# Performance work log

Measured on AMD Instinct MI355X. Metric: run time of the kernel, lower is better.

Reference implementation:

```python
import jax, jax.numpy as jnp
import numpy as np

NUM_ITER = 3  # Newton-Schulz iterations (init kwarg)

def setup_inputs() -> dict:
    key = jax.random.key(0)
    x = jax.random.normal(key, (64, 28, 28, 256), dtype=jnp.float32)
    return {"x": x}

def reference(x):
    B, H, W, C = x.shape
    n = H * W
    # Faithful to K.reshape(inputs, (batch, C, n)) -- a plain row-major reshape
    X = x.reshape(B, C, n)
    # Sigma = X @ I_hat @ X^T with I_hat = (1/n)(I - (1/n) 11^T), i.e. the
    # centering projector: identical to mean-centering then (1/n) Xc Xc^T.
    Xc = X - X.mean(axis=2, keepdims=True)            # [B, C, n]
    Sigma = jnp.einsum('bcn,bdn->bcd', Xc, Xc) / n    # [B, C, C]
    trace = jnp.trace(Sigma, axis1=1, axis2=2)[:, None, None]  # [B,1,1]
    A = Sigma / trace
    I = jnp.eye(C, dtype=x.dtype)
    I3 = 3.0 * I
    Y = A
    Z = jnp.broadcast_to(I, (B, C, C))
    # Newton-Schulz: NOTE original updates Z with the already-updated Y
    for _ in range(NUM_ITER):
        Y = 0.5 * jnp.matmul(Y, I3 - jnp.matmul(Z, Y))
        Z = 0.5 * jnp.matmul(I3 - jnp.matmul(Z, Y), Z)
    Cmat = jnp.sqrt(trace) * Y                        # [B, C, C]
    # Upper-triangular (incl. diagonal) vectorization, row-major order
    iu_r, iu_c = jnp.triu_indices(C)
    return Cmat[:, iu_r, iu_c]                        # [B, C*(C+1)/2]
```

## Files before the change

### kernel.cpp

```cpp
#include <hip/hip_runtime.h>
#include <math.h>

#define BATCH 64
#define CD 256
#define NX 784
#define TRIU_N 32896
#define MSZ 65536
#define REG_STRIDE 1032
#define ARR_STRIDE 4128
#define BUF_STRIDE 16512

typedef unsigned short ushort_t;
typedef unsigned int uint_t;
typedef __attribute__((ext_vector_type(8))) short short8;
typedef __attribute__((ext_vector_type(8))) unsigned short ushort8;
typedef __attribute__((ext_vector_type(16))) float floatx16;

__device__ __forceinline__ ushort_t f2bf(float x) {
    uint_t u = __float_as_uint(x);
    u += 0x7fffu + ((u >> 16) & 1u);
    return (ushort_t)(u >> 16);
}
__device__ __forceinline__ float bf2f(ushort_t h) {
    return __uint_as_float(((uint_t)h) << 16);
}
__device__ __forceinline__ void split2(float x, ushort_t& h, ushort_t& l) {
    h = f2bf(x);
    l = f2bf(x - bf2f(h));
}

__device__ __forceinline__ int swoff(int r, int c) {
    int p = r >> 7, s = (c >> 5) & 7, ks = (c >> 4) & 1, kh = (c >> 3) & 1;
    return ((((p * 8 + s) * 2 + ks) * 2 + kh) * 128 + (r & 127)) * 8 + (c & 7);
}

__device__ __forceinline__ void rawbar() {
    __builtin_amdgcn_s_barrier();
    __builtin_amdgcn_sched_barrier(0);
}

__device__ __forceinline__ void mfma_stage8(const ushort_t* us, int bufbase,
                                            int wr, int wcp, int khalf, int lrow,
                                            floatx16* acc) {
    __builtin_amdgcn_s_setprio(1);
    #pragma unroll
    for (int ks = 0; ks < 2; ++ks) {
        const int rid = ks * 2 + khalf;
        const ushort_t* rb = us + bufbase + rid * REG_STRIDE + lrow * 8;
        short8 aH = *(const short8*)(rb + wr * 256);
        short8 aL = *(const short8*)(rb + ARR_STRIDE + wr * 256);
        #pragma unroll
        for (int cq = 0; cq < 2; ++cq) {
            const int col = wcp * 2 + cq;
            short8 bH = *(const short8*)(rb + 2 * ARR_STRIDE + col * 256);
            short8 bL = *(const short8*)(rb + 3 * ARR_STRIDE + col * 256);
            acc[cq] = __builtin_amdgcn_mfma_f32_32x32x16_bf16(aH, bH, acc[cq], 0, 0, 0);
            acc[cq] = __builtin_amdgcn_mfma_f32_32x32x16_bf16(aH, bL, acc[cq], 0, 0, 0);
            acc[cq] = __builtin_amdgcn_mfma_f32_32x32x16_bf16(aL, bH, acc[cq], 0, 0, 0);
        }
    }
    __builtin_amdgcn_s_setprio(0);
}

__device__ __forceinline__ void acc_bounce(float* fsmem, const floatx16* acc,
                                           int wr, int wcp, int khalf, int lrow) {
    __syncthreads();
    #pragma unroll
    for (int cq = 0; cq < 2; ++cq)
        #pragma unroll
        for (int i = 0; i < 16; ++i) {
            int rl = (i & 3) + ((i >> 2) << 3) + (khalf << 2);
            fsmem[(wr * 32 + rl) * 129 + (wcp * 2 + cq) * 32 + lrow] = acc[cq][i];
        }
    __syncthreads();
}

__global__ __launch_bounds__(512, 1)
void gram_mfma(const float* __restrict__ X, float* __restrict__ means,
               ushort_t* __restrict__ Gh, ushort_t* __restrict__ Gl) {
    __shared__ __align__(16) float fsmem[16512];
    ushort_t* us = (ushort_t*)fsmem;
    const int bb = blockIdx.y, tile = blockIdx.x;
    const int rowBase = (tile >> 1) * 128, colBase = (tile & 1) * 128;
    const int tid = threadIdx.x, lane = tid & 63, wv = tid >> 6;
    const int wr = wv >> 1, wcp = wv & 1;
    const int khalf = lane >> 5, lrow = lane & 31;
    const float* Xb = X + (size_t)bb * CD * NX;

    floatx16 acc[2];
    #pragma unroll
    for (int cq = 0; cq < 2; ++cq)
        #pragma unroll
        for (int i = 0; i < 16; ++i) acc[cq][i] = 0.f;

    int side[2], srow[2], skq[2];
    #pragma unroll
    for (int q = 0; q < 2; ++q) {
        int gid = q * 512 + tid;
        side[q] = gid >> 9;
        srow[q] = (gid >> 2) & 127;
        skq[q]  = gid & 3;
    }
    float rs[2] = {0.f, 0.f};

    float4 cur[2][2];
    #pragma unroll
    for (int q = 0; q < 2; ++q) {
        int gk = skq[q] * 8;
        const float* p = Xb + (size_t)((side[q] ? colBase : rowBase) + srow[q]) * NX + gk;
        cur[q][0] = *(const float4*)p;
        cur[q][1] = *(const float4*)(p + 4);
    }
    #pragma unroll
    for (int q = 0; q < 2; ++q) {
        float f[8] = {cur[q][0].x, cur[q][0].y, cur[q][0].z, cur[q][0].w,
                      cur[q][1].x, cur[q][1].y, cur[q][1].z, cur[q][1].w};
        rs[q] += ((f[0] + f[1]) + (f[2] + f[3])) + ((f[4] + f[5]) + (f[6] + f[7]));
        uint_t hp[4], lp[4];
        #pragma unroll
        for (int i = 0; i < 4; ++i) {
            ushort_t h0, l0, h1, l1;
            split2(f[2*i], h0, l0); split2(f[2*i+1], h1, l1);
            hp[i] = (uint_t)h0 | ((uint_t)h1 << 16);
            lp[i] = (uint_t)l0 | ((uint_t)l1 << 16);
        }
        int base = (side[q] * 2) * ARR_STRIDE + skq[q] * REG_STRIDE + srow[q] * 8;
        *(uint4*)(us + base)              = make_uint4(hp[0], hp[1], hp[2], hp[3]);
        *(uint4*)(us + base + ARR_STRIDE) = make_uint4(lp[0], lp[1], lp[2], lp[3]);
    }

    for (int s = 0; s < 25; ++s) {
        asm volatile("s_waitcnt lgkmcnt(0)" ::: "memory");
        rawbar();
        bool more = (s < 24);
        if (more) {
            #pragma unroll
            for (int q = 0; q < 2; ++q) {
                int gk = (s + 1) * 32 + skq[q] * 8;
                if (gk < NX) {
                    const float* p = Xb + (size_t)((side[q] ? colBase : rowBase) + srow[q]) * NX + gk;
                    cur[q][0] = *(const float4*)p;
                    cur[q][1] = *(const float4*)(p + 4);
                } else {
                    cur[q][0] = make_float4(0.f, 0.f, 0.f, 0.f);
                    cur[q][1] = make_float4(0.f, 0.f, 0.f, 0.f);
                }
            }
        }
        mfma_stage8(us, (s & 1) * BUF_STRIDE, wr, wcp, khalf, lrow, acc);
        if (more) {
            int buf = (s + 1) & 1;
            #pragma unroll
            for (int q = 0; q < 2; ++q) {
                float f[8] = {cur[q][0].x, cur[q][0].y, cur[q][0].z, cur[q][0].w,
                              cur[q][1].x, cur[q][1].y, cur[q][1].z, cur[q][1].w};
                rs[q] += ((f[0] + f[1]) + (f[2] + f[3])) + ((f[4] + f[5]) + (f[6] + f[7]));
                uint_t hp[4], lp[4];
                #pragma unroll
                for (int i = 0; i < 4; ++i) {
                    ushort_t h0, l0, h1, l1;
                    split2(f[2*i], h0, l0); split2(f[2*i+1], h1, l1);
                    hp[i] = (uint_t)h0 | ((uint_t)h1 << 16);
                    lp[i] = (uint_t)l0 | ((uint_t)l1 << 16);
                }
                int base = buf * BUF_STRIDE + (side[q] * 2) * ARR_STRIDE
                         + skq[q] * REG_STRIDE + srow[q] * 8;
                *(uint4*)(us + base)              = make_uint4(hp[0], hp[1], hp[2], hp[3]);
                *(uint4*)(us + base + ARR_STRIDE) = make_uint4(lp[0], lp[1], lp[2], lp[3]);
            }
        }
    }

    {
        float r0 = rs[0], r1 = rs[1];
        r0 += __shfl_xor(r0, 1, 64); r0 += __shfl_xor(r0, 2, 64);
        r1 += __shfl_xor(r1, 1, 64); r1 += __shfl_xor(r1, 2, 64);
        if ((tid & 3) == 0) {
            int rr = tid >> 2;
            means[bb * CD + rowBase + rr] = r0 * (1.0f / NX);
            means[bb * CD + colBase + rr] = r1 * (1.0f / NX);
        }
    }

    acc_bounce(fsmem, acc, wr, wcp, khalf, lrow);
    const int rloc = tid & 127;
    const int r = rowBase + rloc;
    const float mr = means[bb * CD + r];
    #pragma unroll
    for (int gi = 0; gi < 4; ++gi) {
        int g = (tid >> 7) + gi * 4;
        int c0 = colBase + g * 8;
        int so = swoff(r, c0);
        ushort8 hh, ll;
        #pragma unroll
        for (int j = 0; j < 8; ++j) {
            float v = fsmem[rloc * 129 + g * 8 + j] * (1.0f / NX) - mr * means[bb * CD + c0 + j];
            ushort_t h, l; split2(v, h, l);
            hh[j] = h; ll[j] = l;
        }
        *(ushort8*)(Gh + (size_t)bb * MSZ + so) = hh;
        *(ushort8*)(Gl + (size_t)bb * MSZ + so) = ll;
    }
}

__global__ __launch_bounds__(64)
void trace_k(const ushort_t* __restrict__ Gh, const ushort_t* __restrict__ Gl,
             float* __restrict__ itr, float* __restrict__ str_) {
    int b = blockIdx.x, lane = threadIdx.x;
    float s = 0.f;
    #pragma unroll
    for (int i = 0; i < 4; ++i) {
        int c = lane + i * 64;
        size_t d = (size_t)b * MSZ + swoff(c, c);
        s += bf2f(Gh[d]) + bf2f(Gl[d]);
    }
    for (int off = 32; off; off >>= 1) s += __shfl_down(s, off, 64);
    if (lane == 0) { itr[b] = 1.0f / s; str_[b] = sqrtf(s); }
}

__device__ __forceinline__ void ns_prefetch(const ushort_t* const* arrp, ushort_t* us,
                                            int wv, int lane, int s, int buf) {
    #pragma unroll
    for (int j = 0; j < 4; ++j) {
        int ck = wv * 4 + j;
        int arr = ck >> 3, rid = (ck >> 1) & 3, half = ck & 1;
        const ushort_t* g = arrp[arr] + s * 4096 + rid * 1024 + half * 512 + lane * 8;
        ushort_t* l = us + buf * BUF_STRIDE + arr * ARR_STRIDE + rid * REG_STRIDE + half * 512;
        __builtin_amdgcn_global_load_lds(
            (const __attribute__((address_space(1))) unsigned int*)g,
            (__attribute__((address_space(3))) unsigned int*)l, 16, 0, 0);
    }
}

template<int MODE>
__global__ __launch_bounds__(512, 1)
void ns_mfma(const ushort_t* __restrict__ Ah, const ushort_t* __restrict__ Al,
             const ushort_t* __restrict__ Bh, const ushort_t* __restrict__ Bl,
             const ushort_t* __restrict__ Mh, const ushort_t* __restrict__ Ml,
             const float* __restrict__ itr, const float* __restrict__ str_,
             ushort_t* __restrict__ O1h, ushort_t* __restrict__ O1l,
             ushort_t* __restrict__ O2h, ushort_t* __restrict__ O2l,
             float* __restrict__ outT) {
    const int tile = blockIdx.x;
    const int rowBase = (tile >> 1) * 128, colBase = (tile & 1) * 128;
    if (MODE == 3 && rowBase > colBase) return;
    __shared__ __align__(16) float fsmem[33024];
    ushort_t* us = (ushort_t*)fsmem;
    const int bb = blockIdx.y;
    const size_t mb = (size_t)bb * MSZ;
    const int tid = threadIdx.x, lane = tid & 63, wv = tid >> 6;
    const int wr = wv >> 1, wcp = wv & 1;
    const int khalf = lane >> 5, lrow = lane & 31;
    const ushort_t* arrp[4] = {
        Ah + mb + (size_t)(rowBase >> 7) * 32768,
        Al + mb + (size_t)(rowBase >> 7) * 32768,
        Bh + mb + (size_t)(colBase >> 7) * 32768,
        Bl + mb + (size_t)(colBase >> 7) * 32768 };

    floatx16 acc[2];
    #pragma unroll
    for (int cq = 0; cq < 2; ++cq)
        #pragma unroll
        for (int i = 0; i < 16; ++i) acc[cq][i] = 0.f;

    ns_prefetch(arrp, us, wv, lane, 0, 0);
    ns_prefetch(arrp, us, wv, lane, 1, 1);
    ns_prefetch(arrp, us, wv, lane, 2, 2);
    #pragma unroll
    for (int s = 0; s < 8; ++s) {
        if (s <= 5)      asm volatile("s_waitcnt vmcnt(8)" ::: "memory");
        else if (s == 6) asm volatile("s_waitcnt vmcnt(4)" ::: "memory");
        else             asm volatile("s_waitcnt vmcnt(0)" ::: "memory");
        rawbar();
        mfma_stage8(us, (s & 3) * BUF_STRIDE, wr, wcp, khalf, lrow, acc);
        if (s < 5)
            ns_prefetch(arrp, us, wv, lane, s + 3, (s + 3) & 3);
    }

    acc_bounce(fsmem, acc, wr, wcp, khalf, lrow);
    const int rloc = tid & 127;
    const int r = rowBase + rloc;
    float it = 0.f, st = 0.f;
    if (MODE == 2) it = itr[bb];
    if (MODE == 3) st = str_[bb];
    #pragma unroll
    for (int gi = 0; gi < 4; ++gi) {
        int g = (tid >> 7) + gi * 4;
        int c0 = colBase + g * 8;
        int so = swoff(r, c0);
        float v[8];
        #pragma unroll
        for (int j = 0; j < 8; ++j) v[j] = fsmem[rloc * 129 + g * 8 + j];
        if (MODE == 0) {
            ushort8 hh, ll;
            #pragma unroll
            for (int j = 0; j < 8; ++j) {
                ushort_t h, l; split2(v[j], h, l);
                hh[j] = h; ll[j] = l;
            }
            *(ushort8*)(O1h + mb + so) = hh;
            *(ushort8*)(O1l + mb + so) = ll;
        } else {
            ushort8 mh = *(const ushort8*)(Mh + mb + so);
            ushort8 mlv = *(const ushort8*)(Ml + mb + so);
            if (MODE == 1) {
                ushort8 hh, ll;
                #pragma unroll
                for (int j = 0; j < 8; ++j) {
                    float m = bf2f(mh[j]) + bf2f(mlv[j]);
                    float y = fmaf(1.5f, m, -0.5f * v[j]);
                    ushort_t h, l; split2(y, h, l);
                    hh[j] = h; ll[j] = l;
                }
                *(ushort8*)(O1h + mb + so) = hh;
                *(ushort8*)(O1l + mb + so) = ll;
            } else if (MODE == 2) {
                ushort8 yh, yl, zh, zl;
                #pragma unroll
                for (int j = 0; j < 8; ++j) {
                    float m = bf2f(mh[j]) + bf2f(mlv[j]);
                    float y = 1.5f * it * m - 0.5f * it * it * v[j];
                    float z = ((r == c0 + j) ? 1.5f : 0.f) - 0.5f * y;
                    ushort_t h, l;
                    split2(y, h, l); yh[j] = h; yl[j] = l;
                    split2(z, h, l); zh[j] = h; zl[j] = l;
                }
                *(ushort8*)(O1h + mb + so) = yh;
                *(ushort8*)(O1l + mb + so) = yl;
                *(ushort8*)(O2h + mb + so) = zh;
                *(ushort8*)(O2l + mb + so) = zl;
            } else {
                int tb = r * CD - (r * (r - 1)) / 2 - r;
                #pragma unroll
                for (int j = 0; j < 8; ++j) {
                    float m = bf2f(mh[j]) + bf2f(mlv[j]);
                    float y = fmaf(1.5f, m, -0.5f * v[j]);
                    int c = c0 + j;
                    if (c >= r) outT[(size_t)bb * TRIU_N + tb + c] = st * y;
                }
            }
        }
    }
}

extern "C" void kernel_launch(void* const* d_in, const int* in_sizes, int n_in,
                              void* d_out, int out_size, void* d_ws, size_t ws_size,
                              hipStream_t stream) {
    const float* x = (const float*)d_in[0];
    float* out = (float*)d_out;
    char* ws = (char*)d_ws;
    const size_t HS = (size_t)BATCH * MSZ * 2;
    ushort_t* S0h = (ushort_t*)(ws + 0 * HS);
    ushort_t* S0l = (ushort_t*)(ws + 1 * HS);
    ushort_t* S1h = (ushort_t*)(ws + 2 * HS);
    ushort_t* S1l = (ushort_t*)(ws + 3 * HS);
    ushort_t* S2h = (ushort_t*)(ws + 4 * HS);
    ushort_t* S2l = (ushort_t*)(ws + 5 * HS);
    ushort_t* S3h = (ushort_t*)(ws + 6 * HS);
    ushort_t* S3l = (ushort_t*)(ws + 7 * HS);
    float* means = (float*)(ws + 8 * HS);
    float* itr = means + BATCH * CD;
    float* str_ = itr + BATCH;

    dim3 gG(4, BATCH);
    gram_mfma<<<gG, 512, 0, stream>>>(x, means, S0h, S0l);
    trace_k<<<BATCH, 64, 0, stream>>>(S0h, S0l, itr, str_);
    ns_mfma<2><<<gG, 512, 0, stream>>>(S0h, S0l, S0h, S0l, S0h, S0l,
                                       itr, nullptr, S1h, S1l, S2h, S2l, nullptr);
    ns_mfma<0><<<gG, 512, 0, stream>>>(S2h, S2l, S1h, S1l, nullptr, nullptr,
                                       nullptr, nullptr, S3h, S3l, nullptr, nullptr, nullptr);
    ns_mfma<1><<<gG, 512, 0, stream>>>(S1h, S1l, S3h, S3l, S1h, S1l,
                                       nullptr, nullptr, S0h, S0l, nullptr, nullptr, nullptr);
    ns_mfma<0><<<gG, 512, 0, stream>>>(S2h, S2l, S0h, S0l, nullptr, nullptr,
                                       nullptr, nullptr, S3h, S3l, nullptr, nullptr, nullptr);
    ns_mfma<1><<<gG, 512, 0, stream>>>(S3h, S3l, S2h, S2l, S2h, S2l,
                                       nullptr, nullptr, S1h, S1l, nullptr, nullptr, nullptr);
    ns_mfma<0><<<gG, 512, 0, stream>>>(S1h, S1l, S0h, S0l, nullptr, nullptr,
                                       nullptr, nullptr, S3h, S3l, nullptr, nullptr, nullptr);
    ns_mfma<3><<<gG, 512, 0, stream>>>(S0h, S0l, S3h, S3l, S0h, S0l,
                                       nullptr, str_, nullptr, nullptr, nullptr, nullptr, out);
}
```

Before: 245.1 us.

## Load NS fragments directly to registers and double-buffer gram loads two stages ahead

The Newton-Schulz matmul kernel no longer stages tiles through LDS with global_load_lds. Each wave now loads its MFMA operand fragments straight from global memory into registers, using two register sets for double buffering, and shared memory is halved. The gram kernel's loop is unrolled by two with two register staging buffers, so global loads are issued two k-steps ahead. The aim is to cut LDS traffic and barriers and hide more load latency, at the cost of higher register pressure and redundant global reads across waves.

```diff
diff --git a/kernel.cpp b/kernel.cpp
--- a/kernel.cpp
+++ b/kernel.cpp
@@ -73,6 +73,47 @@
             fsmem[(wr * 32 + rl) * 129 + (wcp * 2 + cq) * 32 + lrow] = acc[cq][i];
         }
     __syncthreads();
+}
+
+struct Cur { float4 v[2][2]; };
+
+__device__ __forceinline__ void gr_load(const float* Xb, int rowBase, int colBase, int s,
+                                        const int* side, const int* srow, const int* skq,
+                                        Cur& c) {
+    #pragma unroll
+    for (int q = 0; q < 2; ++q) {
+        int gk = s * 32 + skq[q] * 8;
+        if (gk < NX) {
+            const float* p = Xb + (size_t)((side[q] ? colBase : rowBase) + srow[q]) * NX + gk;
+            c.v[q][0] = *(const float4*)p;
+            c.v[q][1] = *(const float4*)(p + 4);
+        } else {
+            c.v[q][0] = make_float4(0.f, 0.f, 0.f, 0.f);
+            c.v[q][1] = make_float4(0.f, 0.f, 0.f, 0.f);
+        }
+    }
+}
+
+__device__ __forceinline__ void gr_conv(ushort_t* us, int bufbase, const Cur& c,
+                                        const int* side, const int* srow, const int* skq,
+                                        float* rs) {
+    #pragma unroll
+    for (int q = 0; q < 2; ++q) {
+        float f[8] = {c.v[q][0].x, c.v[q][0].y, c.v[q][0].z, c.v[q][0].w,
+                      c.v[q][1].x, c.v[q][1].y, c.v[q][1].z, c.v[q][1].w};
+        rs[q] += ((f[0] + f[1]) + (f[2] + f[3])) + ((f[4] + f[5]) + (f[6] + f[7]));
+        uint_t hp[4], lp[4];
+        #pragma unroll
+        for (int i = 0; i < 4; ++i) {
+            ushort_t h0, l0, h1, l1;
+            split2(f[2*i], h0, l0); split2(f[2*i+1], h1, l1);
+            hp[i] = (uint_t)h0 | ((uint_t)h1 << 16);
+            lp[i] = (uint_t)l0 | ((uint_t)l1 << 16);
+        }
+        int base = bufbase + (side[q] * 2) * ARR_STRIDE + skq[q] * REG_STRIDE + srow[q] * 8;
+        *(uint4*)(us + base)              = make_uint4(hp[0], hp[1], hp[2], hp[3]);
+        *(uint4*)(us + base + ARR_STRIDE) = make_uint4(lp[0], lp[1], lp[2], lp[3]);
+    }
 }
 
 __global__ __launch_bounds__(512, 1)
@@ -103,71 +144,23 @@
     }
     float rs[2] = {0.f, 0.f};
 
-    float4 cur[2][2];
-    #pragma unroll
-    for (int q = 0; q < 2; ++q) {
-        int gk = skq[q] * 8;
-        const float* p = Xb + (size_t)((side[q] ? colBase : rowBase) + srow[q]) * NX + gk;
-        cur[q][0] = *(const float4*)p;
-        cur[q][1] = *(const float4*)(p + 4);
-    }
-    #pragma unroll
-    for (int q = 0; q < 2; ++q) {
-        float f[8] = {cur[q][0].x, cur[q][0].y, cur[q][0].z, cur[q][0].w,
-                      cur[q][1].x, cur[q][1].y, cur[q][1].z, cur[q][1].w};
-        rs[q] += ((f[0] + f[1]) + (f[2] + f[3])) + ((f[4] + f[5]) + (f[6] + f[7]));
-        uint_t hp[4], lp[4];
-        #pragma unroll
-        for (int i = 0; i < 4; ++i) {
-            ushort_t h0, l0, h1, l1;
-            split2(f[2*i], h0, l0); split2(f[2*i+1], h1, l1);
-            hp[i] = (uint_t)h0 | ((uint_t)h1 << 16);
-            lp[i] = (uint_t)l0 | ((uint_t)l1 << 16);
-        }
-        int base = (side[q] * 2) * ARR_STRIDE + skq[q] * REG_STRIDE + srow[q] * 8;
-        *(uint4*)(us + base)              = make_uint4(hp[0], hp[1], hp[2], hp[3]);
-        *(uint4*)(us + base + ARR_STRIDE) = make_uint4(lp[0], lp[1], lp[2], lp[3]);
-    }
-
-    for (int s = 0; s < 25; ++s) {
+    Cur curA, curB;
+    gr_load(Xb, rowBase, colBase, 0, side, srow, skq, curA);
+    gr_load(Xb, rowBase, colBase, 1, side, srow, skq, curB);
+    gr_conv(us, 0, curA, side, srow, skq, rs);
+
+    for (int s = 0; s < 25; s += 2) {
         asm volatile("s_waitcnt lgkmcnt(0)" ::: "memory");
         rawbar();
-        bool more = (s < 24);
-        if (more) {
-            #pragma unroll
-            for (int q = 0; q < 2; ++q) {
-                int gk = (s + 1) * 32 + skq[q] * 8;
-                if (gk < NX) {
-                    const float* p = Xb + (size_t)((side[q] ? colBase : rowBase) + srow[q]) * NX + gk;
-                    cur[q][0] = *(const float4*)p;
-                    cur[q][1] = *(const float4*)(p + 4);
-                } else {
-                    cur[q][0] = make_float4(0.f, 0.f, 0.f, 0.f);
-                    cur[q][1] = make_float4(0.f, 0.f, 0.f, 0.f);
-                }
-            }
-        }
-        mfma_stage8(us, (s & 1) * BUF_STRIDE, wr, wcp, khalf, lrow, acc);
-        if (more) {
-            int buf = (s + 1) & 1;
-            #pragma unroll
-            for (int q = 0; q < 2; ++q) {
-                float f[8] = {cur[q][0].x, cur[q][0].y, cur[q][0].z, cur[q][0].w,
-                              cur[q][1].x, cur[q][1].y, cur[q][1].z, cur[q][1].w};
-                rs[q] += ((f[0] + f[1]) + (f[2] + f[3])) + ((f[4] + f[5]) + (f[6] + f[7]));
-                uint_t hp[4], lp[4];
-                #pragma unroll
-                for (int i = 0; i < 4; ++i) {
-                    ushort_t h0, l0, h1, l1;
-                    split2(f[2*i], h0, l0); split2(f[2*i+1], h1, l1);
-                    hp[i] = (uint_t)h0 | ((uint_t)h1 << 16);
-                    lp[i] = (uint_t)l0 | ((uint_t)l1 << 16);
-                }
-                int base = buf * BUF_STRIDE + (side[q] * 2) * ARR_STRIDE
-                         + skq[q] * REG_STRIDE + srow[q] * 8;
-                *(uint4*)(us + base)              = make_uint4(hp[0], hp[1], hp[2], hp[3]);
-                *(uint4*)(us + base + ARR_STRIDE) = make_uint4(lp[0], lp[1], lp[2], lp[3]);
-            }
+        if (s + 2 <= 24) gr_load(Xb, rowBase, colBase, s + 2, side, srow, skq, curA);
+        mfma_stage8(us, 0, wr, wcp, khalf, lrow, acc);
+        if (s + 1 <= 24) gr_conv(us, BUF_STRIDE, curB, side, srow, skq, rs);
+        if (s + 1 <= 24) {
+            asm volatile("s_waitcnt lgkmcnt(0)" ::: "memory");
+            rawbar();
+            if (s + 3 <= 24) gr_load(Xb, rowBase, colBase, s + 3, side, srow, skq, curB);
+            mfma_stage8(us, BUF_STRIDE, wr, wcp, khalf, lrow, acc);
+            gr_conv(us, 0, curA, side, srow, skq, rs);
         }
     }
 
@@ -218,18 +211,33 @@
     if (lane == 0) { itr[b] = 1.0f / s; str_[b] = sqrtf(s); }
 }
 
-__device__ __forceinline__ void ns_prefetch(const ushort_t* const* arrp, ushort_t* us,
-                                            int wv, int lane, int s, int buf) {
-    #pragma unroll
-    for (int j = 0; j < 4; ++j) {
-        int ck = wv * 4 + j;
-        int arr = ck >> 3, rid = (ck >> 1) & 3, half = ck & 1;
-        const ushort_t* g = arrp[arr] + s * 4096 + rid * 1024 + half * 512 + lane * 8;
-        ushort_t* l = us + buf * BUF_STRIDE + arr * ARR_STRIDE + rid * REG_STRIDE + half * 512;
-        __builtin_amdgcn_global_load_lds(
-            (const __attribute__((address_space(1))) unsigned int*)g,
-            (__attribute__((address_space(3))) unsigned int*)l, 16, 0, 0);
-    }
+__device__ __forceinline__ void ns_ldfr(const ushort_t* aHb, const ushort_t* aLb,
+                                        const ushort_t* bHb, const ushort_t* bLb,
+                                        int s, short8* fa, short8* fb) {
+    #pragma unroll
+    for (int ks = 0; ks < 2; ++ks) {
+        const int off = s * 4096 + ks * 2048;
+        fa[ks * 2 + 0] = *(const short8*)(aHb + off);
+        fa[ks * 2 + 1] = *(const short8*)(aLb + off);
+        #pragma unroll
+        for (int cq = 0; cq < 2; ++cq) {
+            fb[ks * 4 + cq * 2 + 0] = *(const short8*)(bHb + off + cq * 256);
+            fb[ks * 4 + cq * 2 + 1] = *(const short8*)(bLb + off + cq * 256);
+        }
+    }
+}
+
+__device__ __forceinline__ void ns_comp(const short8* fa, const short8* fb, floatx16* acc) {
+    __builtin_amdgcn_s_setprio(1);
+    #pragma unroll
+    for (int ks = 0; ks < 2; ++ks)
+        #pragma unroll
+        for (int cq = 0; cq < 2; ++cq) {
+            acc[cq] = __builtin_amdgcn_mfma_f32_32x32x16_bf16(fa[ks*2+0], fb[ks*4+cq*2+0], acc[cq], 0, 0, 0);
+            acc[cq] = __builtin_amdgcn_mfma_f32_32x32x16_bf16(fa[ks*2+0], fb[ks*4+cq*2+1], acc[cq], 0, 0, 0);
+            acc[cq] = __builtin_amdgcn_mfma_f32_32x32x16_bf16(fa[ks*2+1], fb[ks*4+cq*2+0], acc[cq], 0, 0, 0);
+        }
+    __builtin_amdgcn_s_setprio(0);
 }
 
 template<int MODE>
@@ -244,18 +252,18 @@
     const int tile = blockIdx.x;
     const int rowBase = (tile >> 1) * 128, colBase = (tile & 1) * 128;
     if (MODE == 3 && rowBase > colBase) return;
-    __shared__ __align__(16) float fsmem[33024];
-    ushort_t* us = (ushort_t*)fsmem;
+    __shared__ __align__(16) float fsmem[16512];
     const int bb = blockIdx.y;
     const size_t mb = (size_t)bb * MSZ;
     const int tid = threadIdx.x, lane = tid & 63, wv = tid >> 6;
     const int wr = wv >> 1, wcp = wv & 1;
     const int khalf = lane >> 5, lrow = lane & 31;
-    const ushort_t* arrp[4] = {
-        Ah + mb + (size_t)(rowBase >> 7) * 32768,
-        Al + mb + (size_t)(rowBase >> 7) * 32768,
-        Bh + mb + (size_t)(colBase >> 7) * 32768,
-        Bl + mb + (size_t)(colBase >> 7) * 32768 };
+
+    const int fo = khalf * 1024 + lrow * 8;
+    const ushort_t* aHb = Ah + mb + (size_t)(rowBase >> 7) * 32768 + fo + wr * 256;
+    const ushort_t* aLb = Al + mb + (size_t)(rowBase >> 7) * 32768 + fo + wr * 256;
+    const ushort_t* bHb = Bh + mb + (size_t)(colBase >> 7) * 32768 + fo + (wcp * 2) * 256;
+    const ushort_t* bLb = Bl + mb + (size_t)(colBase >> 7) * 32768 + fo + (wcp * 2) * 256;
 
     floatx16 acc[2];
     #pragma unroll
@@ -263,18 +271,15 @@
         #pragma unroll
         for (int i = 0; i < 16; ++i) acc[cq][i] = 0.f;
 
-    ns_prefetch(arrp, us, wv, lane, 0, 0);
-    ns_prefetch(arrp, us, wv, lane, 1, 1);
-    ns_prefetch(arrp, us, wv, lane, 2, 2);
-    #pragma unroll
-    for (int s = 0; s < 8; ++s) {
-        if (s <= 5)      asm volatile("s_waitcnt vmcnt(8)" ::: "memory");
-        else if (s == 6) asm volatile("s_waitcnt vmcnt(4)" ::: "memory");
-        else             asm volatile("s_waitcnt vmcnt(0)" ::: "memory");
-        rawbar();
-        mfma_stage8(us, (s & 3) * BUF_STRIDE, wr, wcp, khalf, lrow, acc);
-        if (s < 5)
-            ns_prefetch(arrp, us, wv, lane, s + 3, (s + 3) & 3);
+    short8 faA[4], fbA[8], faB[4], fbB[8];
+    ns_ldfr(aHb, aLb, bHb, bLb, 0, faA, fbA);
+    ns_ldfr(aHb, aLb, bHb, bLb, 1, faB, fbB);
+    #pragma unroll
+    for (int s = 0; s < 8; s += 2) {
+        ns_comp(faA, fbA, acc);
+        if (s + 2 < 8) ns_ldfr(aHb, aLb, bHb, bLb, s + 2, faA, fbA);
+        ns_comp(faB, fbB, acc);
+        if (s + 3 < 8) ns_ldfr(aHb, aLb, bHb, bLb, s + 3, faB, fbB);
     }
 
     acc_bounce(fsmem, acc, wr, wcp, khalf, lrow);
```

Result: slower. 267.9 us (+9.3%).
